# Optimization experiments

Hardware: AMD Instinct MI355X
Metric: run time of the kernel (lower is better)

## Reference

```python
import jax, jax.numpy as jnp
import numpy as np

PATCH_SIZE = 3
T = 1.0


def _aggregate_one(v, shift_map, cost_map):
    # v: (C, H, W); shift_map: (2, K, H, W) int; cost_map: (K, H, W)
    p = PATCH_SIZE // 2
    K, H, W = cost_map.shape
    # pad cost with high value (10 -> near-zero softmax weight), shifts with 10 (junk, clamped later)
    pc = jnp.pad(cost_map, ((0, 0), (p, p), (p, p)), constant_values=10.0)
    ps = jnp.pad(shift_map, ((0, 0), (0, 0), (p, p), (p, p)), constant_values=10)
    costs, sis, sjs = [], [], []
    for di in range(PATCH_SIZE):          # small fixed loop (patch_size^2 = 9)
        for dj in range(PATCH_SIZE):
            costs.append(pc[:, di:di + H, dj:dj + W])
            sis.append(ps[0, :, di:di + H, dj:dj + W] + (p - di))
            sjs.append(ps[1, :, di:di + H, dj:dj + W] + (p - dj))
    all_cost = jnp.concatenate(costs, axis=0)                # (P2K, H, W)
    ii = jnp.clip(jnp.concatenate(sis, axis=0), 0, v.shape[1] - 1)
    jj = jnp.clip(jnp.concatenate(sjs, axis=0), 0, v.shape[2] - 1)
    w = jax.nn.softmax(-all_cost / T, axis=0)                # softmax over P2K candidates
    gathered = v[:, ii, jj]                                  # (C, P2K, H, W) irregular gather
    return jnp.sum(w[None] * gathered, axis=1)               # (C, H, W)


def setup_inputs() -> dict:
    key = jax.random.key(0)
    k1, k2, k3 = jax.random.split(key, 3)
    B, C, H, W, K = 2, 32, 256, 256, 4
    v = jax.random.normal(k1, (B, C, H, W), dtype=jnp.float32)
    cost_map = jax.random.uniform(k2, (B, K, H, W), dtype=jnp.float32)
    shift_map = jax.random.randint(k3, (B, 2, K, H, W), 0, H).astype(jnp.int64)
    return {"v": v, "cost_map": cost_map, "shift_map": shift_map}


def reference(v, cost_map, shift_map):
    # Batched PSAttentionMasked.forward with aggregation=True;
    # shift_map/cost_map stand in for the opaque PatchMatch custom kernel output.
    return jax.vmap(_aggregate_one)(v, shift_map, cost_map)
```

## Files before the change

### kernel.cpp

```cpp
#include <hip/hip_runtime.h>
#include <hip/hip_fp16.h>

#define B_ 2
#define C_ 32
#define H_ 256
#define W_ 256
#define K_ 4
#define HW_ (H_ * W_)

__global__ __launch_bounds__(256) void transpose_v_kernel(
    const float* __restrict__ v, __half2* __restrict__ vt) {
  __shared__ float tile[32][65];
  int t = threadIdx.x;
  int pix0 = blockIdx.x * 64;
  int b = pix0 >> 16;
  int pixb = pix0 & (HW_ - 1);
  const float* vb = v + (size_t)b * C_ * HW_;
#pragma unroll
  for (int it = 0; it < 8; ++it) {
    int c = (t >> 6) + it * 4;
    int px = t & 63;
    tile[c][px] = vb[(size_t)c * HW_ + pixb + px];
  }
  __syncthreads();
  __half2* vtb = vt + (size_t)pix0 * (C_ / 2);
#pragma unroll
  for (int it = 0; it < 4; ++it) {
    int px = (t >> 4) + it * 16;
    int c2 = t & 15;
    float lo = tile[2 * c2][px];
    float hi = tile[2 * c2 + 1][px];
    vtb[px * 16 + c2] = __floats2half2_rn(lo, hi);
  }
}

__global__ __launch_bounds__(256, 4) void psatt_kernel(
    const float* __restrict__ cost_map, const int* __restrict__ shift_map,
    const __half2* __restrict__ vt, float* __restrict__ out) {
  __shared__ float lds_e[64][37];
  __shared__ int lds_off[64][37];
  __shared__ float lds_part[64][4];
  __shared__ float lds_inv[64];
  __shared__ float lds_out[64][33];

  int t = threadIdx.x;
  int bid = blockIdx.x;
  int x0 = (bid & 3) << 6;
  int y = (bid >> 2) & (H_ - 1);
  int b = bid >> 10;

  {
    int k = t >> 6;
    int px = t & 63;
    int x = x0 + px;
    const float* cm = cost_map + (size_t)(b * K_ + k) * HW_;
    const int* s0 = shift_map + (size_t)((b * 2 + 0) * K_ + k) * HW_;
    const int* s1 = shift_map + (size_t)((b * 2 + 1) * K_ + k) * HW_;
    float psum = 0.f;
#pragma unroll
    for (int di = 0; di < 3; ++di) {
      int ny = y + di - 1;
      bool yin = (unsigned)ny < (unsigned)H_;
#pragma unroll
      for (int dj = 0; dj < 3; ++dj) {
        int nx = x + dj - 1;
        bool inb = yin && ((unsigned)nx < (unsigned)W_);
        int nidx = ny * W_ + nx;
        float cost;
        int si, sj;
        if (inb) {
          cost = cm[nidx];
          si = s0[nidx] + (1 - di);
          sj = s1[nidx] + (1 - dj);
        } else {
          cost = 10.0f;
          si = 11 - di;
          sj = 11 - dj;
        }
        float e = __expf(-cost);
        int ii = min(max(si, 0), H_ - 1);
        int jj = min(max(sj, 0), W_ - 1);
        int m = k * 9 + di * 3 + dj;
        lds_e[px][m] = e;
        lds_off[px][m] = ii * W_ + jj;
        psum += e;
      }
    }
    lds_part[px][k] = psum;
  }
  __syncthreads();
  if (t < 64) {
    lds_inv[t] =
        1.0f / (lds_part[t][0] + lds_part[t][1] + lds_part[t][2] + lds_part[t][3]);
  }
  __syncthreads();

  {
    int g = t >> 4;
    int c2 = t & 15;
    const __half2* vb = vt + (size_t)b * HW_ * 16 + c2;
#pragma unroll
    for (int rep = 0; rep < 2; ++rep) {
      int pxA = (g << 2) + rep * 2;
      int pxB = pxA + 1;
      float a0 = 0.f, a1 = 0.f, b0 = 0.f, b1 = 0.f;
#pragma unroll
      for (int m = 0; m < 36; ++m) {
        int offA = lds_off[pxA][m];
        int offB = lds_off[pxB][m];
        float eA = lds_e[pxA][m];
        float eB = lds_e[pxB][m];
        __half2 hA = vb[(size_t)offA << 4];
        __half2 hB = vb[(size_t)offB << 4];
        float2 fA = __half22float2(hA);
        float2 fB = __half22float2(hB);
        a0 += eA * fA.x; a1 += eA * fA.y;
        b0 += eB * fB.x; b1 += eB * fB.y;
      }
      float invA = lds_inv[pxA];
      float invB = lds_inv[pxB];
      lds_out[pxA][2 * c2]     = a0 * invA;
      lds_out[pxA][2 * c2 + 1] = a1 * invA;
      lds_out[pxB][2 * c2]     = b0 * invB;
      lds_out[pxB][2 * c2 + 1] = b1 * invB;
    }
  }
  __syncthreads();

  {
    int px = t & 63;
#pragma unroll
    for (int it = 0; it < 8; ++it) {
      int c = (t >> 6) + it * 4;
      out[((size_t)(b * C_ + c) * H_ + y) * W_ + x0 + px] = lds_out[px][c];
    }
  }
}

extern "C" void kernel_launch(void* const* d_in, const int* in_sizes, int n_in,
                              void* d_out, int out_size, void* d_ws, size_t ws_size,
                              hipStream_t stream) {
  const float* v = (const float*)d_in[0];
  const float* cost_map = (const float*)d_in[1];
  const int* shift_map = (const int*)d_in[2];
  float* out = (float*)d_out;

  __half2* vt = (__half2*)d_ws;
  const int grid = B_ * H_ * (W_ / 64);

  transpose_v_kernel<<<B_ * HW_ / 64, 256, 0, stream>>>(v, vt);
  psatt_kernel<<<grid, 256, 0, stream>>>(cost_map, shift_map, vt, out);
}
```

Measured before the change: 47.46 us.

## Remap blocks per XCD, use nontemporal streaming accesses, gather four pixels per thread

Block IDs are remapped so each of the 8 XCDs handles a contiguous slice of one batch, keeping that batch's transposed v table local to one XCD's L2. Streaming loads and stores (v read, vt write, cost/shift loads, output store) are marked nontemporal so they do not evict the gathered vt data from cache. The gather loop now processes four pixels at once with a 9-way unroll, giving more independent loads in flight. The trade-offs are higher register pressure and a dependence on round-robin dispatch of blocks across XCDs.

```diff
diff --git a/kernel.cpp b/kernel.cpp
--- a/kernel.cpp
+++ b/kernel.cpp
@@ -9,7 +9,7 @@
 #define HW_ (H_ * W_)
 
 __global__ __launch_bounds__(256) void transpose_v_kernel(
-    const float* __restrict__ v, __half2* __restrict__ vt) {
+    const float* __restrict__ v, unsigned int* __restrict__ vt) {
   __shared__ float tile[32][65];
   int t = threadIdx.x;
   int pix0 = blockIdx.x * 64;
@@ -20,17 +20,20 @@
   for (int it = 0; it < 8; ++it) {
     int c = (t >> 6) + it * 4;
     int px = t & 63;
-    tile[c][px] = vb[(size_t)c * HW_ + pixb + px];
+    tile[c][px] = __builtin_nontemporal_load(&vb[(size_t)c * HW_ + pixb + px]);
   }
   __syncthreads();
-  __half2* vtb = vt + (size_t)pix0 * (C_ / 2);
+  unsigned int* vtb = vt + (size_t)pix0 * (C_ / 2);
 #pragma unroll
   for (int it = 0; it < 4; ++it) {
     int px = (t >> 4) + it * 16;
     int c2 = t & 15;
     float lo = tile[2 * c2][px];
     float hi = tile[2 * c2 + 1][px];
-    vtb[px * 16 + c2] = __floats2half2_rn(lo, hi);
+    __half2 h = __floats2half2_rn(lo, hi);
+    unsigned int bits;
+    __builtin_memcpy(&bits, &h, 4);
+    __builtin_nontemporal_store(bits, &vtb[px * 16 + c2]);
   }
 }
 
@@ -45,9 +48,12 @@
 
   int t = threadIdx.x;
   int bid = blockIdx.x;
-  int x0 = (bid & 3) << 6;
-  int y = (bid >> 2) & (H_ - 1);
-  int b = bid >> 10;
+  int xcd = bid & 7;
+  int slot = bid >> 3;
+  int b = xcd >> 2;
+  int workid = ((xcd & 3) << 8) + slot;
+  int y = workid >> 2;
+  int x0 = (workid & 3) << 6;
 
   {
     int k = t >> 6;
@@ -69,9 +75,9 @@
         float cost;
         int si, sj;
         if (inb) {
-          cost = cm[nidx];
-          si = s0[nidx] + (1 - di);
-          sj = s1[nidx] + (1 - dj);
+          cost = __builtin_nontemporal_load(&cm[nidx]);
+          si = __builtin_nontemporal_load(&s0[nidx]) + (1 - di);
+          sj = __builtin_nontemporal_load(&s1[nidx]) + (1 - dj);
         } else {
           cost = 10.0f;
           si = 11 - di;
@@ -99,31 +105,34 @@
     int g = t >> 4;
     int c2 = t & 15;
     const __half2* vb = vt + (size_t)b * HW_ * 16 + c2;
-#pragma unroll
-    for (int rep = 0; rep < 2; ++rep) {
-      int pxA = (g << 2) + rep * 2;
-      int pxB = pxA + 1;
-      float a0 = 0.f, a1 = 0.f, b0 = 0.f, b1 = 0.f;
-#pragma unroll
-      for (int m = 0; m < 36; ++m) {
-        int offA = lds_off[pxA][m];
-        int offB = lds_off[pxB][m];
-        float eA = lds_e[pxA][m];
-        float eB = lds_e[pxB][m];
-        __half2 hA = vb[(size_t)offA << 4];
-        __half2 hB = vb[(size_t)offB << 4];
-        float2 fA = __half22float2(hA);
-        float2 fB = __half22float2(hB);
-        a0 += eA * fA.x; a1 += eA * fA.y;
-        b0 += eB * fB.x; b1 += eB * fB.y;
-      }
-      float invA = lds_inv[pxA];
-      float invB = lds_inv[pxB];
-      lds_out[pxA][2 * c2]     = a0 * invA;
-      lds_out[pxA][2 * c2 + 1] = a1 * invA;
-      lds_out[pxB][2 * c2]     = b0 * invB;
-      lds_out[pxB][2 * c2 + 1] = b1 * invB;
+    int px0 = g << 2;
+    float a0x = 0.f, a0y = 0.f, a1x = 0.f, a1y = 0.f;
+    float a2x = 0.f, a2y = 0.f, a3x = 0.f, a3y = 0.f;
+#pragma unroll 9
+    for (int m = 0; m < 36; ++m) {
+      int o0 = lds_off[px0 + 0][m];
+      int o1 = lds_off[px0 + 1][m];
+      int o2 = lds_off[px0 + 2][m];
+      int o3 = lds_off[px0 + 3][m];
+      float e0 = lds_e[px0 + 0][m];
+      float e1 = lds_e[px0 + 1][m];
+      float e2 = lds_e[px0 + 2][m];
+      float e3 = lds_e[px0 + 3][m];
+      float2 f0 = __half22float2(vb[(size_t)o0 << 4]);
+      float2 f1 = __half22float2(vb[(size_t)o1 << 4]);
+      float2 f2 = __half22float2(vb[(size_t)o2 << 4]);
+      float2 f3 = __half22float2(vb[(size_t)o3 << 4]);
+      a0x += e0 * f0.x; a0y += e0 * f0.y;
+      a1x += e1 * f1.x; a1y += e1 * f1.y;
+      a2x += e2 * f2.x; a2y += e2 * f2.y;
+      a3x += e3 * f3.x; a3y += e3 * f3.y;
     }
+    float i0 = lds_inv[px0 + 0], i1 = lds_inv[px0 + 1];
+    float i2 = lds_inv[px0 + 2], i3 = lds_inv[px0 + 3];
+    lds_out[px0 + 0][2 * c2] = a0x * i0; lds_out[px0 + 0][2 * c2 + 1] = a0y * i0;
+    lds_out[px0 + 1][2 * c2] = a1x * i1; lds_out[px0 + 1][2 * c2 + 1] = a1y * i1;
+    lds_out[px0 + 2][2 * c2] = a2x * i2; lds_out[px0 + 2][2 * c2 + 1] = a2y * i2;
+    lds_out[px0 + 3][2 * c2] = a3x * i3; lds_out[px0 + 3][2 * c2 + 1] = a3y * i3;
   }
   __syncthreads();
 
@@ -132,7 +141,9 @@
 #pragma unroll
     for (int it = 0; it < 8; ++it) {
       int c = (t >> 6) + it * 4;
-      out[((size_t)(b * C_ + c) * H_ + y) * W_ + x0 + px] = lds_out[px][c];
+      __builtin_nontemporal_store(
+          lds_out[px][c],
+          &out[((size_t)(b * C_ + c) * H_ + y) * W_ + x0 + px]);
     }
   }
 }
@@ -145,9 +156,10 @@
   const int* shift_map = (const int*)d_in[2];
   float* out = (float*)d_out;
 
-  __half2* vt = (__half2*)d_ws;
+  unsigned int* vt = (unsigned int*)d_ws;
   const int grid = B_ * H_ * (W_ / 64);
 
   transpose_v_kernel<<<B_ * HW_ / 64, 256, 0, stream>>>(v, vt);
-  psatt_kernel<<<grid, 256, 0, stream>>>(cost_map, shift_map, vt, out);
+  psatt_kernel<<<grid, 256, 0, stream>>>(cost_map, shift_map,
+                                         (const __half2*)vt, out);
 }
```

Measured after the change: 56.87 us. +19.8%, slower.
